# Optimization experiments

Measured on AMD Instinct MI355X. Metric: run time of the kernel, lower is better.

Reference implementation:

```python
import jax, jax.numpy as jnp
import numpy as np


def setup_inputs() -> dict:
    key = jax.random.key(0)
    k1, k2 = jax.random.split(key)
    B, C, H, W = 16, 32, 256, 256
    OH, OW = 256, 256
    Im = jax.random.normal(k1, (B, C, H, W), dtype=jnp.float32)
    # pixel-space sampling coordinates in [0, W-1] / [0, H-1]
    gx = jax.random.uniform(k2, (B, 1, OH, OW), dtype=jnp.float32) * (W - 1)
    gy = jax.random.uniform(jax.random.fold_in(k2, 1), (B, 1, OH, OW), dtype=jnp.float32) * (H - 1)
    G = jnp.concatenate([gx, gy], axis=1)  # [B, 2, OH, OW]
    return {"Im": Im, "G": G}


def reference(Im, G):
    # replicate-pad by 1 on each spatial side
    Imp = jnp.pad(Im, ((0, 0), (0, 0), (1, 1), (1, 1)), mode='edge')
    B, C, H, W = Imp.shape
    _, _, OH, OW = G.shape
    # flatten coords per batch; +1 accounts for the pad
    x = G[:, 0].reshape(B, -1) + 1.0  # [B, OH*OW]
    y = G[:, 1].reshape(B, -1) + 1.0
    max_x, max_y = W - 1, H - 1
    x0 = jnp.floor(x).astype(jnp.int32)
    y0 = jnp.floor(y).astype(jnp.int32)
    x1 = x0 + 1
    y1 = y0 + 1
    x0 = jnp.clip(x0, 0, max_x)
    x1 = jnp.clip(x1, 0, max_x)
    y0 = jnp.clip(y0, 0, max_y)
    y1 = jnp.clip(y1, 0, max_y)
    # [B, H*W, C] channels-last flat image, gather per batch
    Im_flat = Imp.transpose(0, 2, 3, 1).reshape(B, H * W, C)

    def gather(yi, xi):
        idx = yi * W + xi  # [B, OH*OW]
        return jnp.take_along_axis(Im_flat, idx[:, :, None], axis=1)  # [B, OH*OW, C]

    Ia = gather(y0, x0)
    Ib = gather(y1, x0)
    Ic = gather(y0, x1)
    Id = gather(y1, x1)
    dx = x1.astype(jnp.float32) - x  # note: uses clamped x1, as in the original
    dy = y1.astype(jnp.float32) - y
    wa = (dy * dx)[:, :, None]
    wb = ((1.0 - dy) * dx)[:, :, None]
    wc = (dy * (1.0 - dx))[:, :, None]
    wd = ((1.0 - dy) * (1.0 - dx))[:, :, None]
    out = wa * Ia + wb * Ib + wc * Ic + wd * Id  # [B, OH*OW, C]
    return out.reshape(B, OH, OW, C).transpose(0, 3, 1, 2)
```

## Files before the change

kernel.cpp:

```cpp
#include <hip/hip_runtime.h>

#define BB 16
#define CC 32
#define HH 256
#define WW 256
#define OHH 256
#define OWW 256
#define HW  (HH * WW)

#define TBLK_HALF (8 * HH * (WW / 64))
#define GBLK_HALF (8 * (HW / 128))
#define MIX_BLOCKS (TBLK_HALF + GBLK_HALF)

typedef _Float16 half8 __attribute__((ext_vector_type(8)));
typedef float float4v __attribute__((ext_vector_type(4)));

__device__ __forceinline__ void transpose_tile(
    const float* __restrict__ Im, _Float16* __restrict__ img,
    int b, int h, int w0, bool nt, float* lds)
{
    int t = threadIdx.x;
    const float* src = Im + ((size_t)b * CC * HH + h) * WW;
    #pragma unroll
    for (int i = 0; i < 2; ++i) {
        int idx = i * 256 + t;
        int c  = idx >> 4;
        int wq = (idx & 15) * 4;
        float4v v = __builtin_nontemporal_load(
            (const float4v*)(src + (size_t)c * HW + w0 + wq));
        lds[(wq + 0) * 33 + c] = v.x;
        lds[(wq + 1) * 33 + c] = v.y;
        lds[(wq + 2) * 33 + c] = v.z;
        lds[(wq + 3) * 33 + c] = v.w;
    }
    __syncthreads();
    int w  = t >> 2;
    int c8 = (t & 3) * 8;
    half8 v;
    #pragma unroll
    for (int j = 0; j < 8; ++j)
        v[j] = (_Float16)lds[w * 33 + c8 + j];
    _Float16* dstp = img + (((size_t)b * HH + h) * WW + w0 + w) * CC + c8;
    if (nt) __builtin_nontemporal_store(v, (half8*)dstp);
    else    *(half8*)dstp = v;
}

__device__ __forceinline__ void gather_unit(
    const _Float16* __restrict__ img, const float* __restrict__ G,
    float* __restrict__ out, int b, int u)
{
    int t    = threadIdx.x;
    int hid  = t & 1;
    int pixb = u * 128 + (t >> 1);

    const float* Gb = G + (size_t)b * 2 * HW + pixb;
    float gx = __builtin_nontemporal_load(Gb);
    float gy = __builtin_nontemporal_load(Gb + HW);

    float x = gx + 1.0f;
    float y = gy + 1.0f;
    int x0 = (int)floorf(x);
    int y0 = (int)floorf(y);
    int x1 = x0 + 1;
    int y1 = y0 + 1;
    x0 = min(max(x0, 0), WW + 1);
    x1 = min(max(x1, 0), WW + 1);
    y0 = min(max(y0, 0), HH + 1);
    y1 = min(max(y1, 0), HH + 1);
    float dx = (float)x1 - x;
    float dy = (float)y1 - y;

    int xi0 = min(max(x0 - 1, 0), WW - 1);
    int xi1 = min(max(x1 - 1, 0), WW - 1);
    int yi0 = min(max(y0 - 1, 0), HH - 1);
    int yi1 = min(max(y1 - 1, 0), HH - 1);

    float wa = dy * dx;
    float wb = (1.0f - dy) * dx;
    float wc = dy * (1.0f - dx);
    float wd = (1.0f - dy) * (1.0f - dx);

    const _Float16* base = img + (size_t)b * HW * CC + hid * 16;
    const half8* pa = (const half8*)(base + ((size_t)yi0 * WW + xi0) * CC);
    const half8* pb = (const half8*)(base + ((size_t)yi1 * WW + xi0) * CC);
    const half8* pc = (const half8*)(base + ((size_t)yi0 * WW + xi1) * CC);
    const half8* pd = (const half8*)(base + ((size_t)yi1 * WW + xi1) * CC);

    half8 a0 = pa[0], a1 = pa[1];
    half8 b0 = pb[0], b1 = pb[1];
    half8 c0 = pc[0], c1 = pc[1];
    half8 d0 = pd[0], d1 = pd[1];

    float r[16];
    #pragma unroll
    for (int j = 0; j < 8; ++j) {
        r[j]     = wa * (float)a0[j] + wb * (float)b0[j]
                 + wc * (float)c0[j] + wd * (float)d0[j];
        r[j + 8] = wa * (float)a1[j] + wb * (float)b1[j]
                 + wc * (float)c1[j] + wd * (float)d1[j];
    }

    float* outp = out + ((size_t)b * CC + hid * 16) * HW + pixb;
    #pragma unroll
    for (int j = 0; j < 16; ++j) {
        __builtin_nontemporal_store(r[j], outp + j * HW);
    }
}

__global__ __launch_bounds__(256) void tpass1(
    const float* __restrict__ Im, _Float16* __restrict__ img)
{
    __shared__ float lds[64 * 33];
    int m = blockIdx.x;
    int b = 8 + (m & 7);
    int slot = m >> 3;
    transpose_tile(Im, img, b, slot >> 2, (slot & 3) * 64, false, lds);
}

__global__ __launch_bounds__(256) void mixpass(
    const float* __restrict__ Im, _Float16* __restrict__ img,
    const float* __restrict__ G, float* __restrict__ out)
{
    __shared__ float lds[64 * 33];
    int m = blockIdx.x;
    int q = m / 24;
    int r = m - q * 24;
    if (r < 8) {
        gather_unit(img, G, out, 8 + r, q);
    } else {
        int xcd = r & 7;
        int ti  = q * 2 + (r >> 4);
        transpose_tile(Im, img, xcd, ti >> 2, (ti & 3) * 64, true, lds);
    }
}

__global__ __launch_bounds__(256) void gpass3(
    const _Float16* __restrict__ img, const float* __restrict__ G,
    float* __restrict__ out)
{
    int m = blockIdx.x;
    gather_unit(img, G, out, m & 7, m >> 3);
}

__global__ __launch_bounds__(256) void bilerp_direct(
    const float* __restrict__ Im, const float* __restrict__ G,
    float* __restrict__ out)
{
    int idx = blockIdx.x * blockDim.x + threadIdx.x;
    int ox = idx & (OWW - 1);
    int oy = (idx >> 8) & (OHH - 1);
    int b  = idx >> 16;

    const float* Gb = G + (size_t)b * 2 * HW + oy * OWW + ox;
    float x = Gb[0] + 1.0f;
    float y = Gb[HW] + 1.0f;
    int x0 = (int)floorf(x), y0 = (int)floorf(y);
    int x1 = x0 + 1, y1 = y0 + 1;
    x0 = min(max(x0, 0), WW + 1); x1 = min(max(x1, 0), WW + 1);
    y0 = min(max(y0, 0), HH + 1); y1 = min(max(y1, 0), HH + 1);
    float dx = (float)x1 - x, dy = (float)y1 - y;
    int xi0 = min(max(x0 - 1, 0), WW - 1), xi1 = min(max(x1 - 1, 0), WW - 1);
    int yi0 = min(max(y0 - 1, 0), HH - 1), yi1 = min(max(y1 - 1, 0), HH - 1);
    float wa = dy * dx, wb = (1.0f - dy) * dx;
    float wc = dy * (1.0f - dx), wd = (1.0f - dy) * (1.0f - dx);

    const float* Ibase = Im + (size_t)b * CC * HW;
    int o00 = yi0 * WW + xi0, o01 = yi0 * WW + xi1;
    int o10 = yi1 * WW + xi0, o11 = yi1 * WW + xi1;
    float* outp = out + (size_t)b * CC * HW + oy * OWW + ox;
    #pragma unroll 4
    for (int c = 0; c < CC; ++c) {
        const float* p = Ibase + c * HW;
        outp[c * HW] = wa * p[o00] + wb * p[o10] + wc * p[o01] + wd * p[o11];
    }
}

extern "C" void kernel_launch(void* const* d_in, const int* in_sizes, int n_in,
                              void* d_out, int out_size, void* d_ws, size_t ws_size,
                              hipStream_t stream) {
    const float* Im = (const float*)d_in[0];
    const float* G  = (const float*)d_in[1];
    float* out = (float*)d_out;

    const size_t needed = (size_t)BB * HW * CC * sizeof(_Float16);
    int total = BB * OHH * OWW;

    if (ws_size >= needed) {
        _Float16* nhwc = (_Float16*)d_ws;
        tpass1 <<<dim3(TBLK_HALF),  dim3(256), 0, stream>>>(Im, nhwc);
        mixpass<<<dim3(MIX_BLOCKS), dim3(256), 0, stream>>>(Im, nhwc, G, out);
        gpass3 <<<dim3(GBLK_HALF),  dim3(256), 0, stream>>>(nhwc, G, out);
    } else {
        bilerp_direct<<<dim3(total / 256), dim3(256), 0, stream>>>(Im, G, out);
    }
}
```

Baseline: 263.8 us.

## Fuse three passes into one persistent cooperative kernel with grid syncs

Replaces the three separate launches (transpose half, mixed gather/transpose, gather half) with a single cooperative kernel of 1024 persistent blocks that loops over the same work items and separates the phases with grid-wide syncs. The goal is to remove per-launch overhead and the idle gaps between kernels. A trailing __syncthreads is added to the transpose tile so LDS can be reused safely across loop iterations. The cost is grid.sync barrier overhead, a fixed block count that may load-balance worse than the original launch-per-item grids, and an extra block barrier per tile. The old three-launch path is kept as a fallback if the cooperative launch fails.

```diff
diff --git a/kernel.cpp b/kernel.cpp
--- a/kernel.cpp
+++ b/kernel.cpp
@@ -1,4 +1,7 @@
 #include <hip/hip_runtime.h>
+#include <hip/hip_cooperative_groups.h>
+
+namespace cg = cooperative_groups;
 
 #define BB 16
 #define CC 32
@@ -10,7 +13,9 @@
 
 #define TBLK_HALF (8 * HH * (WW / 64))
 #define GBLK_HALF (8 * (HW / 128))
-#define MIX_BLOCKS (TBLK_HALF + GBLK_HALF)
+#define MIX_ITEMS (TBLK_HALF + GBLK_HALF)
+
+#define FUSED_BLOCKS 1024
 
 typedef _Float16 half8 __attribute__((ext_vector_type(8)));
 typedef float float4v __attribute__((ext_vector_type(4)));
@@ -43,6 +48,7 @@
     _Float16* dstp = img + (((size_t)b * HH + h) * WW + w0 + w) * CC + c8;
     if (nt) __builtin_nontemporal_store(v, (half8*)dstp);
     else    *(half8*)dstp = v;
+    __syncthreads();
 }
 
 __device__ __forceinline__ void gather_unit(
@@ -107,6 +113,39 @@
     }
 }
 
+__global__ __launch_bounds__(256, 4) void fused(
+    const float* __restrict__ Im, _Float16* __restrict__ img,
+    const float* __restrict__ G, float* __restrict__ out)
+{
+    __shared__ float lds[64 * 33];
+    cg::grid_group grid = cg::this_grid();
+    int nb = gridDim.x;
+
+    for (int i = blockIdx.x; i < TBLK_HALF; i += nb) {
+        int b = 8 + (i & 7);
+        int slot = i >> 3;
+        transpose_tile(Im, img, b, slot >> 2, (slot & 3) * 64, false, lds);
+    }
+    grid.sync();
+
+    for (int i = blockIdx.x; i < MIX_ITEMS; i += nb) {
+        int q = i / 24;
+        int r = i - q * 24;
+        if (r < 8) {
+            gather_unit(img, G, out, 8 + r, q);
+        } else {
+            int xcd = r & 7;
+            int ti  = q * 2 + (r >> 4);
+            transpose_tile(Im, img, xcd, ti >> 2, (ti & 3) * 64, true, lds);
+        }
+    }
+    grid.sync();
+
+    for (int i = blockIdx.x; i < GBLK_HALF; i += nb) {
+        gather_unit(img, G, out, i & 7, i >> 3);
+    }
+}
+
 __global__ __launch_bounds__(256) void tpass1(
     const float* __restrict__ Im, _Float16* __restrict__ img)
 {
@@ -187,9 +226,14 @@
 
     if (ws_size >= needed) {
         _Float16* nhwc = (_Float16*)d_ws;
-        tpass1 <<<dim3(TBLK_HALF),  dim3(256), 0, stream>>>(Im, nhwc);
-        mixpass<<<dim3(MIX_BLOCKS), dim3(256), 0, stream>>>(Im, nhwc, G, out);
-        gpass3 <<<dim3(GBLK_HALF),  dim3(256), 0, stream>>>(nhwc, G, out);
+        void* args[] = { (void*)&Im, (void*)&nhwc, (void*)&G, (void*)&out };
+        hipError_t e = hipLaunchCooperativeKernel(
+            (const void*)fused, dim3(FUSED_BLOCKS), dim3(256), args, 0, stream);
+        if (e != hipSuccess) {
+            tpass1 <<<dim3(TBLK_HALF), dim3(256), 0, stream>>>(Im, nhwc);
+            mixpass<<<dim3(MIX_ITEMS), dim3(256), 0, stream>>>(Im, nhwc, G, out);
+            gpass3 <<<dim3(GBLK_HALF), dim3(256), 0, stream>>>(nhwc, G, out);
+        }
     } else {
         bilerp_direct<<<dim3(total / 256), dim3(256), 0, stream>>>(Im, G, out);
     }
```

Measured after the change: 528.2 us. 100% more time.
